# Kernel optimization log

Hardware: AMD Instinct MI355X
Metric: run time of the kernel (lower is better)

Reference implementation:

```python
import jax, jax.numpy as jnp
import numpy as np

QLEN, MLEN, BSZ, DMODEL, NHEAD, DHEAD = 512, 512, 8, 1024, 16, 64
KLEN = QLEN + MLEN
LN_EPS = 1e-5


def layer_norm(x, g, b):
    mu = jnp.mean(x, axis=-1, keepdims=True)
    var = jnp.var(x, axis=-1, keepdims=True)
    return (x - mu) / jnp.sqrt(var + LN_EPS) * g + b


def rel_shift(x):
    # x: [qlen, klen, bsz, n_head] -- Transformer-XL relative shift trick
    q, k, b, n = x.shape
    x_pad = jnp.pad(x, ((0, 0), (1, 0), (0, 0), (0, 0)))  # zero col at front of dim 1
    x_pad = x_pad.reshape(k + 1, q, b, n)
    return x_pad[1:].reshape(q, k, b, n)


def setup_inputs() -> dict:
    key = jax.random.key(0)
    ks = jax.random.split(key, 10)
    w = lambda k, shape: (jax.random.normal(k, shape, jnp.float32) * 0.02)
    return {
        "content": jax.random.normal(ks[0], (QLEN, BSZ, DMODEL), jnp.float32),
        "mems": jax.random.normal(ks[1], (MLEN, BSZ, DMODEL), jnp.float32),
        "r": jax.random.normal(ks[2], (KLEN, DMODEL), jnp.float32),
        "q_bias": w(ks[3], (NHEAD, DHEAD)),
        "mask": jnp.zeros((QLEN, KLEN, BSZ), jnp.bool_),
        "W_q": w(ks[4], (NHEAD * DHEAD, DMODEL)),
        "W_kv": w(ks[5], (2 * NHEAD * DHEAD, DMODEL)),
        "W_r": w(ks[6], (NHEAD * DHEAD, DMODEL)),
        "b_r": jnp.zeros((NHEAD * DHEAD,), jnp.float32),
        "W_o": w(ks[7], (DMODEL, NHEAD * DHEAD)),
        "b_o": jnp.zeros((DMODEL,), jnp.float32),
        "ln_g": jnp.ones((DMODEL,), jnp.float32),
        "ln_b": jnp.zeros((DMODEL,), jnp.float32),
    }


def reference(content, mems, r, q_bias, mask, W_q, W_kv, W_r, b_r, W_o, b_o, ln_g, ln_b):
    Q, B, D = content.shape
    H, Dh = q_bias.shape
    scale = 1.0 / (Dh ** 0.5)

    c = layer_norm(content, ln_g, ln_b)          # [Q,B,D]
    m = layer_norm(mems, ln_g, ln_b)             # [M,B,D]
    cat = jnp.concatenate([m, c], axis=0)        # [K,B,D]
    K = cat.shape[0]

    kv = cat @ W_kv.T                            # [K,B,2*H*Dh]
    k, v = jnp.split(kv, 2, axis=-1)
    k = k.reshape(K, B, H, Dh)
    v = v.reshape(K, B, H, Dh)

    q = (c @ W_q.T).reshape(Q, B, H, Dh) + q_bias  # [Q,B,H,Dh]
    rproj = (r @ W_r.T + b_r).reshape(K, H, Dh)    # [K,H,Dh]

    AC = jnp.einsum('ibnd,jbnd->ijbn', q, k)       # content-content
    BD = rel_shift(jnp.einsum('ibnd,jnd->ijbn', q, rproj))  # content-position
    score = (AC + BD) * scale                      # [Q,K,B,H]
    score = jnp.where(mask[..., None], -jnp.inf, score)
    prob = jax.nn.softmax(score, axis=1)

    vec = jnp.einsum('ijbn,jbnd->ibnd', prob, v).reshape(Q, B, H * Dh)
    attn_out = vec @ W_o.T + b_o                   # [Q,B,D]
    # IdentityResidualGate: x + relu(y) with x = layer-normed content
    return c + jax.nn.relu(attn_out)
```

## Files before the change

kernel.cpp:

```cpp
#include <hip/hip_runtime.h>
#include <hip/hip_bf16.h>
#include <math.h>

#define QLEN 512
#define MLENC 512
#define KLEN 1024
#define BSZ 8
#define DMODEL 1024
#define NHEAD 16
#define DHEAD 64

typedef __hip_bfloat16 bf16;
typedef unsigned short u16;
typedef unsigned int u32;
typedef __attribute__((ext_vector_type(8))) short s16x8;
typedef __attribute__((ext_vector_type(4))) float f32x4;

#define MFMA16(a, b, c) __builtin_amdgcn_mfma_f32_16x16x32_bf16(a, b, c, 0, 0, 0)

static __device__ __forceinline__ float b2f(bf16 x) { return __bfloat162float(x); }
static __device__ __forceinline__ bf16 f2b(float x) { return __float2bfloat16(x); }
static __device__ __forceinline__ u16 bbu(float x) {
    bf16 h = __float2bfloat16(x);
    return *reinterpret_cast<u16*>(&h);
}

static __device__ __forceinline__ void gl_lds16(const void* g, void* l) {
    __builtin_amdgcn_global_load_lds(
        (const __attribute__((address_space(1))) void*)g,
        (__attribute__((address_space(3))) void*)l, 16, 0, 0);
}

template <int MODE, bool AF32, bool BF32>
static __device__ __forceinline__ void gemm128_dev(const void* __restrict__ Av,
                                                   const void* __restrict__ Bv,
                                                   const float* __restrict__ bias,
                                                   const bf16* __restrict__ resid,
                                                   bf16* __restrict__ Cb,
                                                   float* __restrict__ Cf,
                                                   int m0, int n0, int N,
                                                   short* As, short* Bs) {
    int tid = threadIdx.x;
    int w = tid >> 6, lane = tid & 63, l15 = lane & 15, quad = lane >> 4;
    int wm = w & 1, wn = w >> 1;

    const short* Ab = (const short*)Av;
    const float* Af = (const float*)Av;
    const short* Bb = (const short*)Bv;
    const float* Bf = (const float*)Bv;

    f32x4 acc[4][4];
#pragma unroll
    for (int i = 0; i < 4; ++i)
#pragma unroll
        for (int j = 0; j < 4; ++j) acc[i][j] = (f32x4){0.f, 0.f, 0.f, 0.f};

    for (int kt = 0; kt < 1024; kt += 32) {
        __syncthreads();
        if (!AF32) {
#pragma unroll
            for (int li = 0; li < 2; ++li) {
                int id = (li * 4 + w) * 64 + lane;
                int row = id >> 2, kc = (id & 3) * 8;
                gl_lds16(Ab + ((size_t)(m0 + row) * 1024 + kt + kc),
                         &As[(li * 4 + w) * 512]);
            }
        } else {
            int m = tid >> 1, kc = (tid & 1) * 16;
            const float* src = Af + (size_t)(m0 + m) * 1024 + kt + kc;
            u32* dst = (u32*)&As[m * 32 + kc];
#pragma unroll
            for (int q2 = 0; q2 < 4; ++q2) {
                float4 f = *(const float4*)(src + q2 * 4);
                dst[q2 * 2]     = ((u32)bbu(f.y) << 16) | bbu(f.x);
                dst[q2 * 2 + 1] = ((u32)bbu(f.w) << 16) | bbu(f.z);
            }
        }
        if (!BF32) {
#pragma unroll
            for (int li = 0; li < 2; ++li) {
                int id = (li * 4 + w) * 64 + lane;
                int row = id >> 2, kc = (id & 3) * 8;
                gl_lds16(Bb + ((size_t)(n0 + row) * 1024 + kt + kc),
                         &Bs[(li * 4 + w) * 512]);
            }
        } else {
            int nn = tid >> 1, kc = (tid & 1) * 16;
            const float* src = Bf + (size_t)(n0 + nn) * 1024 + kt + kc;
            u32* dst = (u32*)&Bs[nn * 32 + kc];
#pragma unroll
            for (int q2 = 0; q2 < 4; ++q2) {
                float4 f = *(const float4*)(src + q2 * 4);
                dst[q2 * 2]     = ((u32)bbu(f.y) << 16) | bbu(f.x);
                dst[q2 * 2 + 1] = ((u32)bbu(f.w) << 16) | bbu(f.z);
            }
        }
        __syncthreads();

        s16x8 af[4], bfr[4];
#pragma unroll
        for (int mb = 0; mb < 4; ++mb)
            af[mb] = *(const s16x8*)&As[(wm * 64 + mb * 16 + l15) * 32 + quad * 8];
#pragma unroll
        for (int nb = 0; nb < 4; ++nb)
            bfr[nb] = *(const s16x8*)&Bs[(wn * 64 + nb * 16 + l15) * 32 + quad * 8];
#pragma unroll
        for (int mb = 0; mb < 4; ++mb)
#pragma unroll
            for (int nb = 0; nb < 4; ++nb)
                acc[mb][nb] = MFMA16(af[mb], bfr[nb], acc[mb][nb]);
    }

#pragma unroll
    for (int mb = 0; mb < 4; ++mb) {
#pragma unroll
        for (int nb = 0; nb < 4; ++nb) {
#pragma unroll
            for (int r = 0; r < 4; ++r) {
                int m = m0 + wm * 64 + mb * 16 + quad * 4 + r;
                int col = n0 + wn * 64 + nb * 16 + l15;
                float v = acc[mb][nb][r];
                if (MODE >= 1) v += bias[col];
                if (MODE == 2) {
                    float rv = b2f(resid[(size_t)m * N + col]);
                    Cf[(size_t)m * N + col] = rv + fmaxf(v, 0.f);
                } else {
                    Cb[(size_t)m * N + col] = f2b(v);
                }
            }
        }
    }
}

template <int MODE, bool AF32, bool BF32>
static __device__ __forceinline__ void gemm64_dev(const void* __restrict__ Av,
                                                  const void* __restrict__ Bv,
                                                  const float* __restrict__ bias,
                                                  const bf16* __restrict__ resid,
                                                  bf16* __restrict__ Cb,
                                                  float* __restrict__ Cf,
                                                  int m0, int n0, int N,
                                                  short* As, short* Bs) {
    int tid = threadIdx.x;
    int w = tid >> 6, lane = tid & 63, l15 = lane & 15, quad = lane >> 4;

    const short* Ab = (const short*)Av;
    const float* Af = (const float*)Av;
    const short* Bb = (const short*)Bv;
    const float* Bf = (const float*)Bv;

    f32x4 acc[4][2];
#pragma unroll
    for (int i = 0; i < 4; ++i)
#pragma unroll
        for (int j = 0; j < 2; ++j) acc[i][j] = (f32x4){0.f, 0.f, 0.f, 0.f};

    for (int kt = 0; kt < 1024; kt += 32) {
        __syncthreads();
        if (!AF32) {
            int id = w * 64 + lane;
            int row = id >> 2, kc = (id & 3) * 8;
            gl_lds16(Ab + ((size_t)(m0 + row) * 1024 + kt + kc), &As[w * 512]);
        } else {
            int m = tid >> 2, kc = (tid & 3) * 8;
            const float* src = Af + (size_t)(m0 + m) * 1024 + kt + kc;
            u32* dst = (u32*)&As[m * 32 + kc];
#pragma unroll
            for (int q2 = 0; q2 < 2; ++q2) {
                float4 f = *(const float4*)(src + q2 * 4);
                dst[q2 * 2]     = ((u32)bbu(f.y) << 16) | bbu(f.x);
                dst[q2 * 2 + 1] = ((u32)bbu(f.w) << 16) | bbu(f.z);
            }
        }
        if (!BF32) {
#pragma unroll
            for (int li = 0; li < 2; ++li) {
                int id = (li * 4 + w) * 64 + lane;
                int row = id >> 2, kc = (id & 3) * 8;
                gl_lds16(Bb + ((size_t)(n0 + row) * 1024 + kt + kc),
                         &Bs[(li * 4 + w) * 512]);
            }
        } else {
            int nn = tid >> 1, kc = (tid & 1) * 16;
            const float* src = Bf + (size_t)(n0 + nn) * 1024 + kt + kc;
            u32* dst = (u32*)&Bs[nn * 32 + kc];
#pragma unroll
            for (int q2 = 0; q2 < 4; ++q2) {
                float4 f = *(const float4*)(src + q2 * 4);
                dst[q2 * 2]     = ((u32)bbu(f.y) << 16) | bbu(f.x);
                dst[q2 * 2 + 1] = ((u32)bbu(f.w) << 16) | bbu(f.z);
            }
        }
        __syncthreads();

        s16x8 af[4], bfr[2];
#pragma unroll
        for (int mb = 0; mb < 4; ++mb)
            af[mb] = *(const s16x8*)&As[(mb * 16 + l15) * 32 + quad * 8];
#pragma unroll
        for (int nb = 0; nb < 2; ++nb)
            bfr[nb] = *(const s16x8*)&Bs[(w * 32 + nb * 16 + l15) * 32 + quad * 8];
#pragma unroll
        for (int mb = 0; mb < 4; ++mb)
#pragma unroll
            for (int nb = 0; nb < 2; ++nb)
                acc[mb][nb] = MFMA16(af[mb], bfr[nb], acc[mb][nb]);
    }

#pragma unroll
    for (int mb = 0; mb < 4; ++mb) {
#pragma unroll
        for (int nb = 0; nb < 2; ++nb) {
#pragma unroll
            for (int r = 0; r < 4; ++r) {
                int m = m0 + mb * 16 + quad * 4 + r;
                int col = n0 + w * 32 + nb * 16 + l15;
                float v = acc[mb][nb][r];
                if (MODE >= 1) v += bias[col];
                if (MODE == 2) {
                    float rv = b2f(resid[(size_t)m * N + col]);
                    Cf[(size_t)m * N + col] = rv + fmaxf(v, 0.f);
                } else {
                    Cb[(size_t)m * N + col] = f2b(v);
                }
            }
        }
    }
}

__global__ __launch_bounds__(256) void wconv_kernel(const float* __restrict__ wq,
                                                    const float* __restrict__ wkv,
                                                    const float* __restrict__ wr,
                                                    const float* __restrict__ wo,
                                                    bf16* __restrict__ out) {
    int off = (blockIdx.x * 256 + threadIdx.x) * 8;
    const float* src;
    if (off < 1048576)       src = wq + off;
    else if (off < 3145728)  src = wkv + (off - 1048576);
    else if (off < 4194304)  src = wr + (off - 3145728);
    else                     src = wo + (off - 4194304);
    float4 f0 = *(const float4*)src;
    float4 f1 = *(const float4*)(src + 4);
    s16x8 v;
    v[0] = (short)bbu(f0.x); v[1] = (short)bbu(f0.y);
    v[2] = (short)bbu(f0.z); v[3] = (short)bbu(f0.w);
    v[4] = (short)bbu(f1.x); v[5] = (short)bbu(f1.y);
    v[6] = (short)bbu(f1.z); v[7] = (short)bbu(f1.w);
    *(s16x8*)((short*)out + off) = v;
}

static __device__ __forceinline__ void ln_body(int row, int tid,
                                               const float* __restrict__ content,
                                               const float* __restrict__ mems,
                                               const float* __restrict__ g,
                                               const float* __restrict__ bet,
                                               bf16* __restrict__ cat,
                                               float* red) {
    const float* src = (row < MLENC * BSZ)
        ? mems + (size_t)row * DMODEL
        : content + (size_t)(row - MLENC * BSZ) * DMODEL;

    float x[4];
    float s = 0.f, ss = 0.f;
#pragma unroll
    for (int l = 0; l < 4; ++l) {
        int d = l * 256 + tid;
        x[l] = src[d];
        s += x[l];
        ss += x[l] * x[l];
    }
#pragma unroll
    for (int off = 32; off > 0; off >>= 1) {
        s  += __shfl_xor(s, off);
        ss += __shfl_xor(ss, off);
    }
    int wid = tid >> 6;
    if ((tid & 63) == 0) { red[wid * 2] = s; red[wid * 2 + 1] = ss; }
    __syncthreads();
    s  = red[0] + red[2] + red[4] + red[6];
    ss = red[1] + red[3] + red[5] + red[7];
    float mu  = s * (1.f / DMODEL);
    float var = ss * (1.f / DMODEL) - mu * mu;
    float rs  = rsqrtf(var + 1e-5f);
    bf16* dst = cat + (size_t)row * DMODEL;
#pragma unroll
    for (int l = 0; l < 4; ++l) {
        int d = l * 256 + tid;
        dst[d] = f2b((x[l] - mu) * rs * g[d] + bet[d]);
    }
}

__global__ __launch_bounds__(256) void ln_kernel(const float* __restrict__ content,
                                                 const float* __restrict__ mems,
                                                 const float* __restrict__ g,
                                                 const float* __restrict__ bet,
                                                 bf16* __restrict__ cat) {
    __shared__ float red[8];
    ln_body(blockIdx.x, threadIdx.x, content, mems, g, bet, cat, red);
}

__global__ __launch_bounds__(256) void prep_kernel(const float* __restrict__ content,
                                                   const float* __restrict__ mems,
                                                   const float* __restrict__ g,
                                                   const float* __restrict__ bet,
                                                   bf16* __restrict__ cat,
                                                   const float* __restrict__ wq,
                                                   const float* __restrict__ wkv,
                                                   const float* __restrict__ wr,
                                                   const float* __restrict__ wo,
                                                   bf16* __restrict__ wout) {
    __shared__ float red[8];
    int bid = blockIdx.x;
    if (bid < KLEN * BSZ) {
        ln_body(bid, threadIdx.x, content, mems, g, bet, cat, red);
    } else {
        int off = ((bid - KLEN * BSZ) * 256 + threadIdx.x) * 8;
        const float* src;
        if (off < 1048576)       src = wq + off;
        else if (off < 3145728)  src = wkv + (off - 1048576);
        else if (off < 4194304)  src = wr + (off - 3145728);
        else                     src = wo + (off - 4194304);
        float4 f0 = *(const float4*)src;
        float4 f1 = *(const float4*)(src + 4);
        s16x8 v;
        v[0] = (short)bbu(f0.x); v[1] = (short)bbu(f0.y);
        v[2] = (short)bbu(f0.z); v[3] = (short)bbu(f0.w);
        v[4] = (short)bbu(f1.x); v[5] = (short)bbu(f1.y);
        v[6] = (short)bbu(f1.z); v[7] = (short)bbu(f1.w);
        *(s16x8*)((short*)wout + off) = v;
    }
}

template <int MODE, bool AF32, bool BF32>
__global__ __launch_bounds__(256) void gemm_mfma(const void* __restrict__ Av,
                                                 const void* __restrict__ Bv,
                                                 const float* __restrict__ bias,
                                                 const bf16* __restrict__ resid,
                                                 bf16* __restrict__ Cb,
                                                 float* __restrict__ Cf,
                                                 int Mr, int N) {
    __shared__ short As[128 * 32];
    __shared__ short Bs[128 * 32];
    gemm128_dev<MODE, AF32, BF32>(Av, Bv, bias, resid, Cb, Cf,
                                  blockIdx.y * 128, blockIdx.x * 128, N, As, Bs);
}

template <int MODE, bool AF32, bool BF32>
__global__ __launch_bounds__(256) void gemm64(const void* __restrict__ Av,
                                              const void* __restrict__ Bv,
                                              const float* __restrict__ bias,
                                              const bf16* __restrict__ resid,
                                              bf16* __restrict__ Cb,
                                              float* __restrict__ Cf,
                                              int Mr, int N) {
    __shared__ short As[64 * 32];
    __shared__ short Bs[128 * 32];
    gemm64_dev<MODE, AF32, BF32>(Av, Bv, bias, resid, Cb, Cf,
                                 blockIdx.y * 64, blockIdx.x * 128, N, As, Bs);
}

__global__ __launch_bounds__(256) void gemms_fused(const bf16* __restrict__ cat,
                                                   const bf16* __restrict__ catc,
                                                   const float* __restrict__ rin,
                                                   const bf16* __restrict__ Wkvb,
                                                   const bf16* __restrict__ Wqb,
                                                   const bf16* __restrict__ Wrb,
                                                   const float* __restrict__ q_bias,
                                                   const float* __restrict__ b_r,
                                                   bf16* __restrict__ kvout,
                                                   bf16* __restrict__ qbout,
                                                   bf16* __restrict__ rpout) {
    __shared__ short As[128 * 32];
    __shared__ short Bs[128 * 32];
    int id = blockIdx.x;
    if (id < 1024) {
        gemm128_dev<0, false, false>(cat, Wkvb, nullptr, nullptr, kvout, nullptr,
                                     (id >> 4) * 128, (id & 15) * 128, 2048, As, Bs);
    } else if (id < 1536) {
        int q = id - 1024;
        gemm64_dev<1, false, false>(catc, Wqb, q_bias, nullptr, qbout, nullptr,
                                    (q >> 3) * 64, (q & 7) * 128, 1024, As, Bs);
    } else {
        int q = id - 1536;
        gemm64_dev<1, true, false>(rin, Wrb, b_r, nullptr, rpout, nullptr,
                                   (q >> 3) * 64, (q & 7) * 128, 1024, As, Bs);
    }
}

__global__ __launch_bounds__(256, 2) void attn_mfma(const bf16* __restrict__ qb,
                                                    const bf16* __restrict__ kv,
                                                    const bf16* __restrict__ rp,
                                                    bf16* __restrict__ vec) {
    __shared__ u16 Ks[64][72];
    __shared__ u16 Vr[2][4096];
    __shared__ u16 Vt[64][72];
    __shared__ u16 Ps[4][16][76];
    __shared__ float Ms[4][16][84];

    int bid = blockIdx.x;
    int it = bid & 7, n = (bid >> 3) & 15, b = bid >> 7;
    int i0 = it * 64;
    int tid = threadIdx.x;
    int w = tid >> 6, lane = tid & 63, l15 = lane & 15, quad = lane >> 4;

    const short* qs = (const short*)qb;
    const short* kvs = (const short*)kv;
    const short* rs = (const short*)rp;

    size_t qoff = (((size_t)(i0 + w * 16 + l15) * 8) + b) * 1024 + n * 64 + quad * 8;
    s16x8 aq0 = *(const s16x8*)(qs + qoff);
    s16x8 aq1 = *(const s16x8*)(qs + qoff + 32);
    int qrow1 = i0 + w * 16 + l15 + 1; if (qrow1 > 511) qrow1 = 511;
    size_t qoffs = (((size_t)qrow1 * 8) + b) * 1024 + n * 64 + quad * 8;
    s16x8 as0 = *(const s16x8*)(qs + qoffs);
    s16x8 as1 = *(const s16x8*)(qs + qoffs + 32);

    f32x4 O0 = {0.f,0.f,0.f,0.f}, O1 = O0, O2 = O0, O3 = O0;
    f32x4 Lacc = O0;
    float mrun[4];
#pragma unroll
    for (int r = 0; r < 4; ++r) mrun[r] = -INFINITY;

    f32x4 z = (f32x4){0.f, 0.f, 0.f, 0.f};
    int ibase = i0 + w * 16 + quad * 4;

    s16x8 ones;
#pragma unroll
    for (int i = 0; i < 8; ++i) ones[i] = (short)0x3F80;

    int r0K = tid >> 3, c0K = (tid & 7) * 8;
    int dV = lane, jV = w * 16;
    int wrow = (3 - w) * 16 + l15;

    auto loadW = [&](int ubase, s16x8* dst) {
#pragma unroll
        for (int ntl = 0; ntl < 5; ++ntl) {
            int u = ubase + wrow + ntl * 16;
            u = u < 0 ? 0 : (u > 1023 ? 1023 : u);
            const short* p = rs + (size_t)u * 1024 + n * 64 + quad * 8;
            dst[ntl * 2]     = *(const s16x8*)p;
            dst[ntl * 2 + 1] = *(const s16x8*)(p + 32);
        }
    };
    auto bandM = [&](const s16x8* wf, s16x8 a0, s16x8 a1, f32x4* th) {
        f32x4 m[5];
#pragma unroll
        for (int ntl = 0; ntl < 5; ++ntl) {
            m[ntl] = MFMA16(a0, wf[ntl * 2], z);
            m[ntl] = MFMA16(a1, wf[ntl * 2 + 1], m[ntl]);
        }
#pragma unroll
        for (int ntl = 0; ntl < 5; ++ntl)
#pragma unroll
            for (int r = 0; r < 4; ++r)
                Ms[w][quad * 4 + r][ntl * 16 + l15] = m[ntl][r];
#pragma unroll
        for (int r = 0; r < 4; ++r) {
            int lr = quad * 4 + r;
            int cb = l15 - lr + 15;
#pragma unroll
            for (int h = 0; h < 4; ++h)
                th[h][r] = Ms[w][lr][cb + 16 * h];
        }
    };

    bool need1c, need2c;
    auto step = [&](int st, s16x8* wcur, s16x8* wnxt) {
        int p = st & 1;
        int j0 = st * 64;
        int d0 = j0 - i0;
        int j0n = (j0 + 64) & 1023;

        __syncthreads();

        size_t base0 = ((size_t)((j0n + r0K) * 8 + b)) * 2048 + n * 64 + c0K;
        size_t base1 = ((size_t)((j0n + 32 + r0K) * 8 + b)) * 2048 + n * 64 + c0K;
        s16x8 kr0 = *(const s16x8*)(kvs + base0);
        s16x8 kr1 = *(const s16x8*)(kvs + base1);
        gl_lds16(kvs + base0 + 1024, &Vr[1 - p][w * 512]);
        gl_lds16(kvs + base1 + 1024, &Vr[1 - p][2048 + w * 512]);

        int d0p = d0 + 64;
        bool need1n = (d0p <= 512);
        bool need2n = (d0p >= 512);
        loadW(need1n ? (448 + d0p) : (d0p - 577), wnxt);

        {
            s16x8 vv0, vv1;
#pragma unroll
            for (int q2 = 0; q2 < 8; ++q2) vv0[q2] = (short)Vr[p][(jV + q2) * 64 + dV];
#pragma unroll
            for (int q2 = 0; q2 < 8; ++q2) vv1[q2] = (short)Vr[p][(jV + 8 + q2) * 64 + dV];
            *(s16x8*)&Vt[dV][jV] = vv0;
            *(s16x8*)&Vt[dV][jV + 8] = vv1;
        }

        f32x4 sc[4];
#pragma unroll
        for (int h = 0; h < 4; ++h) {
            s16x8 bk0 = *(const s16x8*)&Ks[h * 16 + l15][quad * 8];
            s16x8 bk1 = *(const s16x8*)&Ks[h * 16 + l15][32 + quad * 8];
            sc[h] = MFMA16(aq0, bk0, z);
            sc[h] = MFMA16(aq1, bk1, sc[h]);
        }

        f32x4 th1[4], th2[4];
#pragma unroll
        for (int h = 0; h < 4; ++h) { th1[h] = z; th2[h] = z; }
        if (need1c) bandM(wcur, aq0, aq1, th1);
        if (need2c) {
            if (need1c) {
                s16x8 w2[10];
                loadW(d0 - 577, w2);
                bandM(w2, as0, as1, th2);
            } else {
                bandM(wcur, as0, as1, th2);
            }
        }

#pragma unroll
        for (int r = 0; r < 4; ++r) {
            int rr = w * 16 + quad * 4 + r;
            int djb = j0 + l15 - i0 - rr;
#pragma unroll
            for (int h = 0; h < 4; ++h) {
                int dj = djb + 16 * h;
                float bd = (dj <= 512) ? th1[h][r] : ((dj == 513) ? 0.f : th2[h][r]);
                sc[h][r] = (sc[h][r] + bd) * 0.125f;
            }
        }

#pragma unroll
        for (int r = 0; r < 4; ++r) {
            float ml = fmaxf(fmaxf(sc[0][r], sc[1][r]), fmaxf(sc[2][r], sc[3][r]));
            ml = fmaxf(ml, __shfl_xor(ml, 1));
            ml = fmaxf(ml, __shfl_xor(ml, 2));
            ml = fmaxf(ml, __shfl_xor(ml, 4));
            ml = fmaxf(ml, __shfl_xor(ml, 8));
            float mn = fmaxf(mrun[r], ml);
            float p0 = __expf(sc[0][r] - mn);
            float p1 = __expf(sc[1][r] - mn);
            float p2 = __expf(sc[2][r] - mn);
            float p3 = __expf(sc[3][r] - mn);
            float al = __expf(mrun[r] - mn);
            mrun[r] = mn;
            Lacc[r] *= al;
            O0[r] *= al; O1[r] *= al; O2[r] *= al; O3[r] *= al;
            int lr = quad * 4 + r;
            Ps[w][lr][l15]      = bbu(p0);
            Ps[w][lr][16 + l15] = bbu(p1);
            Ps[w][lr][32 + l15] = bbu(p2);
            Ps[w][lr][48 + l15] = bbu(p3);
        }

        __syncthreads();

        s16x8 ap0 = *(const s16x8*)&Ps[w][l15][quad * 8];
        s16x8 ap1 = *(const s16x8*)&Ps[w][l15][32 + quad * 8];
        {
            s16x8 bv0 = *(const s16x8*)&Vt[l15][quad * 8];
            s16x8 bv1 = *(const s16x8*)&Vt[l15][32 + quad * 8];
            O0 = MFMA16(ap0, bv0, O0);
            O0 = MFMA16(ap1, bv1, O0);
        }
        {
            s16x8 bv0 = *(const s16x8*)&Vt[16 + l15][quad * 8];
            s16x8 bv1 = *(const s16x8*)&Vt[16 + l15][32 + quad * 8];
            O1 = MFMA16(ap0, bv0, O1);
            O1 = MFMA16(ap1, bv1, O1);
        }
        {
            s16x8 bv0 = *(const s16x8*)&Vt[32 + l15][quad * 8];
            s16x8 bv1 = *(const s16x8*)&Vt[32 + l15][32 + quad * 8];
            O2 = MFMA16(ap0, bv0, O2);
            O2 = MFMA16(ap1, bv1, O2);
        }
        {
            s16x8 bv0 = *(const s16x8*)&Vt[48 + l15][quad * 8];
            s16x8 bv1 = *(const s16x8*)&Vt[48 + l15][32 + quad * 8];
            O3 = MFMA16(ap0, bv0, O3);
            O3 = MFMA16(ap1, bv1, O3);
        }
        Lacc = MFMA16(ap0, ones, Lacc);
        Lacc = MFMA16(ap1, ones, Lacc);

        *(s16x8*)&Ks[r0K][c0K] = kr0;
        *(s16x8*)&Ks[32 + r0K][c0K] = kr1;
        need1c = need1n;
        need2c = need2n;
    };

    s16x8 wA[10], wB[10];
    {
        size_t base0 = ((size_t)(r0K * 8 + b)) * 2048 + n * 64 + c0K;
        size_t base1 = ((size_t)((32 + r0K) * 8 + b)) * 2048 + n * 64 + c0K;
        s16x8 k0 = *(const s16x8*)(kvs + base0);
        s16x8 k1 = *(const s16x8*)(kvs + base1);
        gl_lds16(kvs + base0 + 1024, &Vr[0][w * 512]);
        gl_lds16(kvs + base1 + 1024, &Vr[0][2048 + w * 512]);
        *(s16x8*)&Ks[r0K][c0K] = k0;
        *(s16x8*)&Ks[32 + r0K][c0K] = k1;
        loadW(448 - i0, wA);
        need1c = true;
        need2c = (-i0 >= 512);
    }

    for (int st2 = 0; st2 < 16; st2 += 2) {
        step(st2,     wA, wB);
        step(st2 + 1, wB, wA);
    }

#pragma unroll
    for (int r = 0; r < 4; ++r) {
        float inv = 1.f / Lacc[r];
        int ig = ibase + r;
        size_t o = ((size_t)ig * 8 + b) * 1024 + n * 64;
        vec[o + l15]      = f2b(O0[r] * inv);
        vec[o + 16 + l15] = f2b(O1[r] * inv);
        vec[o + 32 + l15] = f2b(O2[r] * inv);
        vec[o + 48 + l15] = f2b(O3[r] * inv);
    }
}

extern "C" void kernel_launch(void* const* d_in, const int* in_sizes, int n_in,
                              void* d_out, int out_size, void* d_ws, size_t ws_size,
                              hipStream_t stream) {
    const float* content = (const float*)d_in[0];
    const float* mems    = (const float*)d_in[1];
    const float* r       = (const float*)d_in[2];
    const float* q_bias  = (const float*)d_in[3];
    const float* W_q     = (const float*)d_in[5];
    const float* W_kv    = (const float*)d_in[6];
    const float* W_r     = (const float*)d_in[7];
    const float* b_r     = (const float*)d_in[8];
    const float* W_o     = (const float*)d_in[9];
    const float* b_o     = (const float*)d_in[10];
    const float* ln_g    = (const float*)d_in[11];
    const float* ln_b    = (const float*)d_in[12];

    bf16* ws   = (bf16*)d_ws;
    bf16* cat  = ws;
    bf16* kv   = cat + 8388608;
    bf16* qb   = kv + 16777216;
    bf16* rp   = qb + 4194304;
    bf16* vecb = rp + 1048576;
    bf16* Wb   = vecb + 4194304;
    bf16* catc = cat + (size_t)MLENC * BSZ * DMODEL;

    bf16* Wqb  = Wb;
    bf16* Wkvb = Wb + 1048576;
    bf16* Wrb  = Wb + 3145728;
    bf16* Wob  = Wb + 4194304;

    const size_t FULLW_BYTES = (size_t)(34603008 + 5242880) * 2;
    bool fullw = ws_size >= FULLW_BYTES;

    if (fullw) {
        prep_kernel<<<KLEN * BSZ + 2560, 256, 0, stream>>>(
            content, mems, ln_g, ln_b, cat, W_q, W_kv, W_r, W_o, Wb);

        gemms_fused<<<1664, 256, 0, stream>>>(
            cat, catc, r, Wkvb, Wqb, Wrb, q_bias, b_r, kv, qb, rp);
    } else {
        ln_kernel<<<KLEN * BSZ, 256, 0, stream>>>(content, mems, ln_g, ln_b, cat);
        gemm_mfma<0, false, true><<<dim3(16, 64), 256, 0, stream>>>(
            cat, W_kv, nullptr, nullptr, kv, nullptr, 8192, 2048);
        gemm64<1, false, true><<<dim3(8, 64), 256, 0, stream>>>(
            catc, W_q, q_bias, nullptr, qb, nullptr, 4096, 1024);
        gemm64<1, true, true><<<dim3(8, 16), 256, 0, stream>>>(
            r, W_r, b_r, nullptr, rp, nullptr, 1024, 1024);
    }

    attn_mfma<<<BSZ * NHEAD * 8, 256, 0, stream>>>(qb, kv, rp, vecb);

    if (fullw) {
        gemm64<2, false, false><<<dim3(8, 64), 256, 0, stream>>>(
            vecb, Wob, b_o, catc, nullptr, (float*)d_out, 4096, 1024);
    } else {
        gemm64<2, false, true><<<dim3(8, 64), 256, 0, stream>>>(
            vecb, W_o, b_o, catc, nullptr, (float*)d_out, 4096, 1024);
    }
}
```

Before: 346.0 us.

## Double GEMM K-tile to 64 with XOR-swizzled LDS and lazy softmax rescale

The GEMM device functions now stage K=64 per iteration instead of 32, halving the barrier and loop count, and lay out LDS with an XOR swizzle on 8-element chunks to avoid bank conflicts on the fragment reads. LDS buffers double in size. The attention softmax skips the running-max rescale of O and L unless the new max exceeds the old by more than a threshold, which saves exp and multiply work but lets probabilities grow up to e^8 before rescaling. An unused weight-conversion kernel is also removed.

```diff
diff --git a/kernel.cpp b/kernel.cpp
--- a/kernel.cpp
+++ b/kernel.cpp
@@ -23,6 +23,9 @@
 static __device__ __forceinline__ u16 bbu(float x) {
     bf16 h = __float2bfloat16(x);
     return *reinterpret_cast<u16*>(&h);
+}
+static __device__ __forceinline__ u32 pk2(float a, float b) {
+    return ((u32)bbu(b) << 16) | bbu(a);
 }
 
 static __device__ __forceinline__ void gl_lds16(const void* g, void* l) {
@@ -55,60 +58,78 @@
 #pragma unroll
         for (int j = 0; j < 4; ++j) acc[i][j] = (f32x4){0.f, 0.f, 0.f, 0.f};
 
-    for (int kt = 0; kt < 1024; kt += 32) {
+    for (int kt = 0; kt < 1024; kt += 64) {
         __syncthreads();
         if (!AF32) {
 #pragma unroll
-            for (int li = 0; li < 2; ++li) {
+            for (int li = 0; li < 4; ++li) {
                 int id = (li * 4 + w) * 64 + lane;
-                int row = id >> 2, kc = (id & 3) * 8;
+                int row = id >> 3;
+                int kc = ((id & 7) ^ (row & 7)) * 8;
                 gl_lds16(Ab + ((size_t)(m0 + row) * 1024 + kt + kc),
                          &As[(li * 4 + w) * 512]);
             }
         } else {
-            int m = tid >> 1, kc = (tid & 1) * 16;
-            const float* src = Af + (size_t)(m0 + m) * 1024 + kt + kc;
-            u32* dst = (u32*)&As[m * 32 + kc];
-#pragma unroll
-            for (int q2 = 0; q2 < 4; ++q2) {
-                float4 f = *(const float4*)(src + q2 * 4);
-                dst[q2 * 2]     = ((u32)bbu(f.y) << 16) | bbu(f.x);
-                dst[q2 * 2 + 1] = ((u32)bbu(f.w) << 16) | bbu(f.z);
+            int m = tid >> 1, kcl = (tid & 1) * 32;
+            const float* src = Af + (size_t)(m0 + m) * 1024 + kt + kcl;
+#pragma unroll
+            for (int ch = 0; ch < 4; ++ch) {
+                int cl = (kcl >> 3) + ch;
+                u32* dst = (u32*)&As[m * 64 + ((cl ^ (m & 7)) * 8)];
+                float4 f0 = *(const float4*)(src + ch * 8);
+                float4 f1 = *(const float4*)(src + ch * 8 + 4);
+                dst[0] = pk2(f0.x, f0.y); dst[1] = pk2(f0.z, f0.w);
+                dst[2] = pk2(f1.x, f1.y); dst[3] = pk2(f1.z, f1.w);
             }
         }
         if (!BF32) {
 #pragma unroll
-            for (int li = 0; li < 2; ++li) {
+            for (int li = 0; li < 4; ++li) {
                 int id = (li * 4 + w) * 64 + lane;
-                int row = id >> 2, kc = (id & 3) * 8;
+                int row = id >> 3;
+                int kc = ((id & 7) ^ (row & 7)) * 8;
                 gl_lds16(Bb + ((size_t)(n0 + row) * 1024 + kt + kc),
                          &Bs[(li * 4 + w) * 512]);
             }
         } else {
-            int nn = tid >> 1, kc = (tid & 1) * 16;
-            const float* src = Bf + (size_t)(n0 + nn) * 1024 + kt + kc;
-            u32* dst = (u32*)&Bs[nn * 32 + kc];
-#pragma unroll
-            for (int q2 = 0; q2 < 4; ++q2) {
-                float4 f = *(const float4*)(src + q2 * 4);
-                dst[q2 * 2]     = ((u32)bbu(f.y) << 16) | bbu(f.x);
-                dst[q2 * 2 + 1] = ((u32)bbu(f.w) << 16) | bbu(f.z);
+            int nn = tid >> 1, kcl = (tid & 1) * 32;
+            const float* src = Bf + (size_t)(n0 + nn) * 1024 + kt + kcl;
+#pragma unroll
+            for (int ch = 0; ch < 4; ++ch) {
+                int cl = (kcl >> 3) + ch;
+                u32* dst = (u32*)&Bs[nn * 64 + ((cl ^ (nn & 7)) * 8)];
+                float4 f0 = *(const float4*)(src + ch * 8);
+                float4 f1 = *(const float4*)(src + ch * 8 + 4);
+                dst[0] = pk2(f0.x, f0.y); dst[1] = pk2(f0.z, f0.w);
+                dst[2] = pk2(f1.x, f1.y); dst[3] = pk2(f1.z, f1.w);
             }
         }
         __syncthreads();
 
-        s16x8 af[4], bfr[4];
+        s16x8 af[4][2], bfr[4][2];
+#pragma unroll
+        for (int mb = 0; mb < 4; ++mb) {
+            int row = wm * 64 + mb * 16 + l15;
+#pragma unroll
+            for (int kh = 0; kh < 2; ++kh)
+                af[mb][kh] = *(const s16x8*)
+                    &As[row * 64 + (((kh * 4 + quad) ^ (row & 7)) * 8)];
+        }
+#pragma unroll
+        for (int nb = 0; nb < 4; ++nb) {
+            int row = wn * 64 + nb * 16 + l15;
+#pragma unroll
+            for (int kh = 0; kh < 2; ++kh)
+                bfr[nb][kh] = *(const s16x8*)
+                    &Bs[row * 64 + (((kh * 4 + quad) ^ (row & 7)) * 8)];
+        }
 #pragma unroll
         for (int mb = 0; mb < 4; ++mb)
-            af[mb] = *(const s16x8*)&As[(wm * 64 + mb * 16 + l15) * 32 + quad * 8];
-#pragma unroll
-        for (int nb = 0; nb < 4; ++nb)
-            bfr[nb] = *(const s16x8*)&Bs[(wn * 64 + nb * 16 + l15) * 32 + quad * 8];
-#pragma unroll
-        for (int mb = 0; mb < 4; ++mb)
-#pragma unroll
-            for (int nb = 0; nb < 4; ++nb)
-                acc[mb][nb] = MFMA16(af[mb], bfr[nb], acc[mb][nb]);
+#pragma unroll
+            for (int nb = 0; nb < 4; ++nb) {
+                acc[mb][nb] = MFMA16(af[mb][0], bfr[nb][0], acc[mb][nb]);
+                acc[mb][nb] = MFMA16(af[mb][1], bfr[nb][1], acc[mb][nb]);
+            }
     }
 
 #pragma unroll
@@ -155,56 +176,78 @@
 #pragma unroll
         for (int j = 0; j < 2; ++j) acc[i][j] = (f32x4){0.f, 0.f, 0.f, 0.f};
 
-    for (int kt = 0; kt < 1024; kt += 32) {
+    for (int kt = 0; kt < 1024; kt += 64) {
         __syncthreads();
         if (!AF32) {
-            int id = w * 64 + lane;
-            int row = id >> 2, kc = (id & 3) * 8;
-            gl_lds16(Ab + ((size_t)(m0 + row) * 1024 + kt + kc), &As[w * 512]);
-        } else {
-            int m = tid >> 2, kc = (tid & 3) * 8;
-            const float* src = Af + (size_t)(m0 + m) * 1024 + kt + kc;
-            u32* dst = (u32*)&As[m * 32 + kc];
-#pragma unroll
-            for (int q2 = 0; q2 < 2; ++q2) {
-                float4 f = *(const float4*)(src + q2 * 4);
-                dst[q2 * 2]     = ((u32)bbu(f.y) << 16) | bbu(f.x);
-                dst[q2 * 2 + 1] = ((u32)bbu(f.w) << 16) | bbu(f.z);
-            }
-        }
-        if (!BF32) {
 #pragma unroll
             for (int li = 0; li < 2; ++li) {
                 int id = (li * 4 + w) * 64 + lane;
-                int row = id >> 2, kc = (id & 3) * 8;
+                int row = id >> 3;
+                int kc = ((id & 7) ^ (row & 7)) * 8;
+                gl_lds16(Ab + ((size_t)(m0 + row) * 1024 + kt + kc),
+                         &As[(li * 4 + w) * 512]);
+            }
+        } else {
+            int m = tid >> 2, kcl = (tid & 3) * 16;
+            const float* src = Af + (size_t)(m0 + m) * 1024 + kt + kcl;
+#pragma unroll
+            for (int ch = 0; ch < 2; ++ch) {
+                int cl = (kcl >> 3) + ch;
+                u32* dst = (u32*)&As[m * 64 + ((cl ^ (m & 7)) * 8)];
+                float4 f0 = *(const float4*)(src + ch * 8);
+                float4 f1 = *(const float4*)(src + ch * 8 + 4);
+                dst[0] = pk2(f0.x, f0.y); dst[1] = pk2(f0.z, f0.w);
+                dst[2] = pk2(f1.x, f1.y); dst[3] = pk2(f1.z, f1.w);
+            }
+        }
+        if (!BF32) {
+#pragma unroll
+            for (int li = 0; li < 4; ++li) {
+                int id = (li * 4 + w) * 64 + lane;
+                int row = id >> 3;
+                int kc = ((id & 7) ^ (row & 7)) * 8;
                 gl_lds16(Bb + ((size_t)(n0 + row) * 1024 + kt + kc),
                          &Bs[(li * 4 + w) * 512]);
             }
         } else {
-            int nn = tid >> 1, kc = (tid & 1) * 16;
-            const float* src = Bf + (size_t)(n0 + nn) * 1024 + kt + kc;
-            u32* dst = (u32*)&Bs[nn * 32 + kc];
-#pragma unroll
-            for (int q2 = 0; q2 < 4; ++q2) {
-                float4 f = *(const float4*)(src + q2 * 4);
-                dst[q2 * 2]     = ((u32)bbu(f.y) << 16) | bbu(f.x);
-                dst[q2 * 2 + 1] = ((u32)bbu(f.w) << 16) | bbu(f.z);
+            int nn = tid >> 1, kcl = (tid & 1) * 32;
+            const float* src = Bf + (size_t)(n0 + nn) * 1024 + kt + kcl;
+#pragma unroll
+            for (int ch = 0; ch < 4; ++ch) {
+                int cl = (kcl >> 3) + ch;
+                u32* dst = (u32*)&Bs[nn * 64 + ((cl ^ (nn & 7)) * 8)];
+                float4 f0 = *(const float4*)(src + ch * 8);
+                float4 f1 = *(const float4*)(src + ch * 8 + 4);
+                dst[0] = pk2(f0.x, f0.y); dst[1] = pk2(f0.z, f0.w);
+                dst[2] = pk2(f1.x, f1.y); dst[3] = pk2(f1.z, f1.w);
             }
         }
         __syncthreads();
 
-        s16x8 af[4], bfr[2];
+        s16x8 af[4][2], bfr[2][2];
+#pragma unroll
+        for (int mb = 0; mb < 4; ++mb) {
+            int row = mb * 16 + l15;
+#pragma unroll
+            for (int kh = 0; kh < 2; ++kh)
+                af[mb][kh] = *(const s16x8*)
+                    &As[row * 64 + (((kh * 4 + quad) ^ (row & 7)) * 8)];
+        }
+#pragma unroll
+        for (int nb = 0; nb < 2; ++nb) {
+            int row = w * 32 + nb * 16 + l15;
+#pragma unroll
+            for (int kh = 0; kh < 2; ++kh)
+                bfr[nb][kh] = *(const s16x8*)
+                    &Bs[row * 64 + (((kh * 4 + quad) ^ (row & 7)) * 8)];
+        }
 #pragma unroll
         for (int mb = 0; mb < 4; ++mb)
-            af[mb] = *(const s16x8*)&As[(mb * 16 + l15) * 32 + quad * 8];
-#pragma unroll
-        for (int nb = 0; nb < 2; ++nb)
-            bfr[nb] = *(const s16x8*)&Bs[(w * 32 + nb * 16 + l15) * 32 + quad * 8];
-#pragma unroll
-        for (int mb = 0; mb < 4; ++mb)
-#pragma unroll
-            for (int nb = 0; nb < 2; ++nb)
-                acc[mb][nb] = MFMA16(af[mb], bfr[nb], acc[mb][nb]);
+#pragma unroll
+            for (int nb = 0; nb < 2; ++nb) {
+                acc[mb][nb] = MFMA16(af[mb][0], bfr[nb][0], acc[mb][nb]);
+                acc[mb][nb] = MFMA16(af[mb][1], bfr[nb][1], acc[mb][nb]);
+            }
     }
 
 #pragma unroll
@@ -226,27 +269,6 @@
             }
         }
     }
-}
-
-__global__ __launch_bounds__(256) void wconv_kernel(const float* __restrict__ wq,
-                                                    const float* __restrict__ wkv,
-                                                    const float* __restrict__ wr,
-                                                    const float* __restrict__ wo,
-                                                    bf16* __restrict__ out) {
-    int off = (blockIdx.x * 256 + threadIdx.x) * 8;
-    const float* src;
-    if (off < 1048576)       src = wq + off;
-    else if (off < 3145728)  src = wkv + (off - 1048576);
-    else if (off < 4194304)  src = wr + (off - 3145728);
-    else                     src = wo + (off - 4194304);
-    float4 f0 = *(const float4*)src;
-    float4 f1 = *(const float4*)(src + 4);
-    s16x8 v;
-    v[0] = (short)bbu(f0.x); v[1] = (short)bbu(f0.y);
-    v[2] = (short)bbu(f0.z); v[3] = (short)bbu(f0.w);
-    v[4] = (short)bbu(f1.x); v[5] = (short)bbu(f1.y);
-    v[6] = (short)bbu(f1.z); v[7] = (short)bbu(f1.w);
-    *(s16x8*)((short*)out + off) = v;
 }
 
 static __device__ __forceinline__ void ln_body(int row, int tid,
@@ -339,8 +361,8 @@
                                                  bf16* __restrict__ Cb,
                                                  float* __restrict__ Cf,
                                                  int Mr, int N) {
-    __shared__ short As[128 * 32];
-    __shared__ short Bs[128 * 32];
+    __shared__ short As[128 * 64];
+    __shared__ short Bs[128 * 64];
     gemm128_dev<MODE, AF32, BF32>(Av, Bv, bias, resid, Cb, Cf,
                                   blockIdx.y * 128, blockIdx.x * 128, N, As, Bs);
 }
@@ -353,8 +375,8 @@
                                               bf16* __restrict__ Cb,
                                               float* __restrict__ Cf,
                                               int Mr, int N) {
-    __shared__ short As[64 * 32];
-    __shared__ short Bs[128 * 32];
+    __shared__ short As[64 * 64];
+    __shared__ short Bs[128 * 64];
     gemm64_dev<MODE, AF32, BF32>(Av, Bv, bias, resid, Cb, Cf,
                                  blockIdx.y * 64, blockIdx.x * 128, N, As, Bs);
 }
@@ -370,8 +392,8 @@
                                                    bf16* __restrict__ kvout,
                                                    bf16* __restrict__ qbout,
                                                    bf16* __restrict__ rpout) {
-    __shared__ short As[128 * 32];
-    __shared__ short Bs[128 * 32];
+    __shared__ short As[128 * 64];
+    __shared__ short Bs[128 * 64];
     int id = blockIdx.x;
     if (id < 1024) {
         gemm128_dev<0, false, false>(cat, Wkvb, nullptr, nullptr, kvout, nullptr,
@@ -537,15 +559,17 @@
             ml = fmaxf(ml, __shfl_xor(ml, 2));
             ml = fmaxf(ml, __shfl_xor(ml, 4));
             ml = fmaxf(ml, __shfl_xor(ml, 8));
-            float mn = fmaxf(mrun[r], ml);
-            float p0 = __expf(sc[0][r] - mn);
-            float p1 = __expf(sc[1][r] - mn);
-            float p2 = __expf(sc[2][r] - mn);
-            float p3 = __expf(sc[3][r] - mn);
-            float al = __expf(mrun[r] - mn);
-            mrun[r] = mn;
-            Lacc[r] *= al;
-            O0[r] *= al; O1[r] *= al; O2[r] *= al; O3[r] *= al;
+            if (__any(ml > mrun[r] + 8.f)) {
+                float mn = fmaxf(mrun[r], ml);
+                float al = __expf(mrun[r] - mn);
+                mrun[r] = mn;
+                Lacc[r] *= al;
+                O0[r] *= al; O1[r] *= al; O2[r] *= al; O3[r] *= al;
+            }
+            float p0 = __expf(sc[0][r] - mrun[r]);
+            float p1 = __expf(sc[1][r] - mrun[r]);
+            float p2 = __expf(sc[2][r] - mrun[r]);
+            float p3 = __expf(sc[3][r] - mrun[r]);
             int lr = quad * 4 + r;
             Ps[w][lr][l15]      = bbu(p0);
             Ps[w][lr][16 + l15] = bbu(p1);
```

New measurement: 337.0 us. -2.6%, faster.
